# Kernel optimization log

Measured on AMD Instinct MI355X. Metric: run time of the kernel, lower is better.

The kernel has to match this reference:

```python
import jax, jax.numpy as jnp
import numpy as np
from jax import lax

B, NUM_HEADS, DIM_C, DIM_V = 8, 8, 768, 768
H = W = 56
HEAD_DIM = DIM_V // NUM_HEADS  # 96
STRIDE_Q = (1, 1)
STRIDE_KV = (2, 2)
REL_DIM = 2 * H - 1  # 111


def _ln(x, g, b, eps=1e-5):
    m = jnp.mean(x, axis=-1, keepdims=True)
    v = jnp.var(x, axis=-1, keepdims=True)
    return (x - m) * lax.rsqrt(v + eps) * g + b


def _pool(t, w, g, b, hw, stride):
    # t: [B, nH, 1+H*W, C]; depthwise 3x3 conv pooling (padding 1), cls token bypasses conv,
    # LayerNorm applied to the full (cls + pooled) tensor, matching attention_pool.
    cls_tok, sp = t[:, :, :1], t[:, :, 1:]
    b_, nh, L, c = sp.shape
    h, wdt = hw
    sp = sp.reshape(b_ * nh, h, wdt, c)
    sp = lax.conv_general_dilated(sp, w, stride, [(1, 1), (1, 1)],
                                  dimension_numbers=('NHWC', 'HWIO', 'NHWC'),
                                  feature_group_count=c)
    ho, wo = sp.shape[1], sp.shape[2]
    sp = sp.reshape(b_, nh, ho * wo, c)
    out = _ln(jnp.concatenate([cls_tok, sp], axis=2), g, b)
    return out, (ho, wo)


def _rel_idx(q_s, k_s):
    q_ratio = max(k_s / q_s, 1.0)
    k_ratio = max(q_s / k_s, 1.0)
    d = np.arange(q_s)[:, None] * q_ratio - np.arange(k_s)[None, :] * k_ratio + (k_s - 1) * k_ratio
    return d.astype(np.int64)


def setup_inputs() -> dict:
    key = jax.random.key(0)
    ks = jax.random.split(key, 8)
    N = H * W + 1
    return {
        'x': jax.random.normal(ks[0], (B, N, DIM_C), jnp.float32),
        'qkv_w': jax.random.normal(ks[1], (DIM_C, 3 * DIM_V), jnp.float32) * 0.02,
        'qkv_b': jnp.zeros((3 * DIM_V,), jnp.float32),
        'pool_q_w': jax.random.normal(ks[2], (3, 3, 1, HEAD_DIM), jnp.float32) * 0.1,
        'pool_k_w': jax.random.normal(ks[3], (3, 3, 1, HEAD_DIM), jnp.float32) * 0.1,
        'pool_v_w': jax.random.normal(ks[4], (3, 3, 1, HEAD_DIM), jnp.float32) * 0.1,
        'nq_g': jnp.ones((HEAD_DIM,), jnp.float32), 'nq_b': jnp.zeros((HEAD_DIM,), jnp.float32),
        'nk_g': jnp.ones((HEAD_DIM,), jnp.float32), 'nk_b': jnp.zeros((HEAD_DIM,), jnp.float32),
        'nv_g': jnp.ones((HEAD_DIM,), jnp.float32), 'nv_b': jnp.zeros((HEAD_DIM,), jnp.float32),
        'rel_pos_h': jax.random.normal(ks[5], (REL_DIM, HEAD_DIM), jnp.float32) * 0.02,
        'rel_pos_w': jax.random.normal(ks[6], (REL_DIM, HEAD_DIM), jnp.float32) * 0.02,
        'hw_h': H,
        'hw_w': W,
    }


def reference(x, qkv_w, qkv_b, pool_q_w, pool_k_w, pool_v_w,
              nq_g, nq_b, nk_g, nk_b, nv_g, nv_b,
              rel_pos_h, rel_pos_w, hw_h, hw_w):
    b, n, _ = x.shape
    qkv = (x @ qkv_w + qkv_b).reshape(b, n, 3, NUM_HEADS, HEAD_DIM).transpose(2, 0, 3, 1, 4)
    q, k, v = qkv[0], qkv[1], qkv[2]  # each [B, nH, N, head_dim]
    q, q_shape = _pool(q, pool_q_w, nq_g, nq_b, (hw_h, hw_w), STRIDE_Q)
    k, k_shape = _pool(k, pool_k_w, nk_g, nk_b, (hw_h, hw_w), STRIDE_KV)
    v, _ = _pool(v, pool_v_w, nv_g, nv_b, (hw_h, hw_w), STRIDE_KV)
    scale = HEAD_DIM ** -0.5
    attn = jnp.einsum('bhqc,bhkc->bhqk', q * scale, k)  # [B, nH, Nq, Nk]
    qh, qw = q_shape
    kh, kw = k_shape
    Rh = rel_pos_h[_rel_idx(qh, kh)]  # [qh, kh, C]
    Rw = rel_pos_w[_rel_idx(qw, kw)]  # [qw, kw, C]
    r_q = q[:, :, 1:].reshape(b, NUM_HEADS, qh, qw, HEAD_DIM)
    rel_h = jnp.einsum('byhwc,hkc->byhwk', r_q, Rh)
    rel_w = jnp.einsum('byhwc,wkc->byhwk', r_q, Rw)
    sp = attn[:, :, 1:, 1:].reshape(b, NUM_HEADS, qh, qw, kh, kw)
    sp = sp + rel_h[..., None] + rel_w[..., None, :]
    attn = attn.at[:, :, 1:, 1:].set(sp.reshape(b, NUM_HEADS, qh * qw, kh * kw))
    attn = jax.nn.softmax(attn, axis=-1)
    out = jnp.einsum('bhqk,bhkc->bhqc', attn, v)
    out = out + q  # residual pooling
    return out.transpose(0, 2, 1, 3).reshape(b, -1, DIM_V)
```

## Files before the change

### kernel.cpp

```cpp
#include <hip/hip_runtime.h>
#include <hip/hip_bf16.h>

typedef __hip_bfloat16 bf16;
typedef __attribute__((ext_vector_type(8))) short s16x8;
typedef __attribute__((ext_vector_type(4))) short s16x4;
typedef __attribute__((ext_vector_type(4))) float f32x4;

#define BATCH 8
#define NH 8
#define NTOK 3137
#define HD 96
#define HH 56
#define WW 56
#define NKEY 785
#define DIMC 768
#define DIM3 2304
#define MROWS (BATCH * NTOK)

__device__ __forceinline__ float b2f(bf16 x) { return __bfloat162float(x); }
__device__ __forceinline__ bf16 f2b(float x) { return __float2bfloat16(x); }
__device__ __forceinline__ float s2f(short s) {
  return __uint_as_float(((uint32_t)(uint16_t)s) << 16);
}
__device__ __forceinline__ short f2bs(float x) {
  bf16 h = __float2bfloat16(x);
  short s; __builtin_memcpy(&s, &h, 2); return s;
}
__device__ __forceinline__ void gload_lds16(const void* g, void* l) {
  __builtin_amdgcn_global_load_lds(
      (const __attribute__((address_space(1))) void*)g,
      (__attribute__((address_space(3))) void*)l, 16, 0, 0);
}
__device__ __forceinline__ int xcd_swz(int bid, int nwg) {
  int q = nwg >> 3, r = nwg & 7;
  int xcd = bid & 7, idx = bid >> 3;
  return (xcd < r ? xcd * (q + 1) : r * (q + 1) + (xcd - r) * q) + idx;
}

__global__ __launch_bounds__(256) void k_cvtX(const float* __restrict__ X,
                                              bf16* __restrict__ Xb, int n4) {
  for (int i = blockIdx.x * blockDim.x + threadIdx.x; i < n4;
       i += gridDim.x * blockDim.x) {
    float4 v = reinterpret_cast<const float4*>(X)[i];
    ushort4 o;
    o.x = (unsigned short)f2bs(v.x); o.y = (unsigned short)f2bs(v.y);
    o.z = (unsigned short)f2bs(v.z); o.w = (unsigned short)f2bs(v.w);
    reinterpret_cast<ushort4*>(Xb)[i] = o;
  }
}

__global__ __launch_bounds__(256) void k_cvtW(const float* __restrict__ W,
                                              bf16* __restrict__ WbT) {
  __shared__ float T[64][65];
  const int n0 = blockIdx.x * 64;
  const int k0 = blockIdx.y * 64;
  const int tid = threadIdx.x;
#pragma unroll
  for (int i = 0; i < 16; i++) {
    int e = tid + i * 256;
    int r = e >> 6, c = e & 63;
    T[r][c] = W[(size_t)(k0 + r) * DIM3 + n0 + c];
  }
  __syncthreads();
#pragma unroll
  for (int i = 0; i < 16; i++) {
    int e = tid + i * 256;
    int r = e >> 6, c = e & 63;
    WbT[(size_t)(n0 + r) * DIMC + k0 + c] = f2b(T[c][r]);
  }
}

__global__ __launch_bounds__(256) void k_cvtRel(const float* __restrict__ relHt,
                                                const float* __restrict__ relWt,
                                                bf16* __restrict__ Brel) {
  int i = blockIdx.x * 256 + threadIdx.x;
  if (i >= 5376) return;
  int elem = i * 4;
  int row = elem / HD, c = elem % HD;
  float4 v = {0.f, 0.f, 0.f, 0.f};
  if (row < 111) v = *(const float4*)(relHt + (size_t)row * HD + c);
  else if (row >= 112 && row < 223) v = *(const float4*)(relWt + (size_t)(row - 112) * HD + c);
  short4 o;
  o.x = f2bs(v.x); o.y = f2bs(v.y); o.z = f2bs(v.z); o.w = f2bs(v.w);
  *(short4*)((short*)Brel + elem) = o;
}

#define QKV_NBX 18
#define QKV_NBY 197
#define QKV_NWG (QKV_NBX * QKV_NBY)

__global__ __launch_bounds__(256, 4) void k_qkv_mfma(
    const bf16* __restrict__ Xb, const bf16* __restrict__ WbT,
    const float* __restrict__ bias,
    bf16* __restrict__ Q, bf16* __restrict__ K, bf16* __restrict__ V) {
  __shared__ __align__(16) short LB[17408];
  const int tid = threadIdx.x;
  const int wid = tid >> 6, lane = tid & 63;
  const int g = lane >> 4, kl = lane & 15;
  const int wm = wid >> 1, wn = wid & 1;
  const int lin = xcd_swz(blockIdx.x, QKV_NWG);
  const int row0 = (lin / QKV_NBX) * 128;
  const int col0 = (lin % QKV_NBX) * 128;

  auto stage = [&](int k0, int buf) {
#pragma unroll
    for (int r = 0; r < 2; r++) {
      int slotb = r * 256 + wid * 64;
      int slot = slotb + lane;
      int sg = slot >> 7, sm = slot & 127;
      int mm = row0 + sm; if (mm > MROWS - 1) mm = MROWS - 1;
      gload_lds16(Xb + (size_t)mm * DIMC + k0 + sg * 8, &LB[buf * 4096 + (slotb << 3)]);
      gload_lds16(WbT + (size_t)(col0 + sm) * DIMC + k0 + sg * 8,
                  &LB[8192 + buf * 4096 + (slotb << 3)]);
    }
  };

  f32x4 acc[4][4] = {};

  stage(0, 0);
  __syncthreads();

  for (int it = 0; it < 24; it++) {
    const int buf = it & 1;
    if (it < 23) stage((it + 1) * 32, buf ^ 1);

    s16x8 af[4], bf[4];
#pragma unroll
    for (int i = 0; i < 4; i++)
      af[i] = *(const s16x8*)&LB[buf * 4096 + (((g << 7) + wm * 64 + i * 16 + kl) << 3)];
#pragma unroll
    for (int j = 0; j < 4; j++)
      bf[j] = *(const s16x8*)&LB[8192 + buf * 4096 + (((g << 7) + wn * 64 + j * 16 + kl) << 3)];
    __builtin_amdgcn_s_setprio(1);
#pragma unroll
    for (int i = 0; i < 4; i++)
#pragma unroll
      for (int j = 0; j < 4; j++)
        acc[i][j] = __builtin_amdgcn_mfma_f32_16x16x32_bf16(af[i], bf[j], acc[i][j], 0, 0, 0);
    __builtin_amdgcn_s_setprio(0);
    __syncthreads();
  }

#pragma unroll
  for (int i = 0; i < 4; i++)
#pragma unroll
    for (int j = 0; j < 4; j++) {
      int n = wn * 64 + j * 16 + kl;
      float bv = bias[col0 + n];
#pragma unroll
      for (int r = 0; r < 4; r++) {
        int m = wm * 64 + i * 16 + g * 4 + r;
        LB[m * 136 + n] = f2bs(acc[i][j][r] + bv);
      }
    }
  __syncthreads();
#pragma unroll
  for (int cc8 = 0; cc8 < 8; cc8++) {
    int ch = tid + cc8 * 256;
    int m = ch >> 4, cc = ch & 15;
    int M = row0 + m;
    if (M < MROWS) {
      int ncol = col0 + cc * 8;
      int s = ncol / DIMC, rr = ncol % DIMC;
      int h = rr / HD, c = rr % HD;
      int b = M / NTOK, nt = M % NTOK;
      bf16* dst = (s == 0) ? Q : (s == 1) ? K : V;
      *(uint4*)(dst + (((size_t)b * NH + h) * NTOK + nt) * HD + c) =
          *(const uint4*)&LB[m * 136 + cc * 8];
    }
  }
}

template <int STRIDE, int OH_, int OW_>
__global__ __launch_bounds__(256) void k_pool(
    const bf16* __restrict__ raw, const float* __restrict__ wgt,
    const float* __restrict__ gam, const float* __restrict__ bet,
    bf16* __restrict__ out) {
  const int ntok = OH_ * OW_ + 1;
  const int ngrp = (ntok + 3) / 4;
  const int bid = xcd_swz(blockIdx.x, 64 * ngrp);
  const int grp = bid % ngrp;
  const int bh = bid / ngrp;
  const int wid = threadIdx.x >> 6, lane = threadIdx.x & 63;
  const int t = grp * 4 + wid;
  if (t >= ntok) return;
  const bf16* src = raw + (size_t)bh * NTOK * HD;
  const int c2 = lane * 2;

  float v0 = 0.f, v1 = 0.f;
  if (lane < 48) {
    if (t == 0) {
      ushort2 u = *(const ushort2*)(src + c2);
      v0 = s2f((short)u.x); v1 = s2f((short)u.y);
    } else {
      int oy = (t - 1) / OW_, ox = (t - 1) % OW_;
#pragma unroll
      for (int dy = 0; dy < 3; dy++) {
        int iy = oy * STRIDE + dy - 1;
        if (iy < 0 || iy >= HH) continue;
#pragma unroll
        for (int dx = 0; dx < 3; dx++) {
          int ix = ox * STRIDE + dx - 1;
          if (ix < 0 || ix >= WW) continue;
          ushort2 u = *(const ushort2*)(src + (size_t)(1 + iy * WW + ix) * HD + c2);
          float2 w = *(const float2*)(wgt + (dy * 3 + dx) * HD + c2);
          v0 += s2f((short)u.x) * w.x;
          v1 += s2f((short)u.y) * w.y;
        }
      }
    }
  }
  float s = v0 + v1;
  float s2 = v0 * v0 + v1 * v1;
#pragma unroll
  for (int o = 32; o > 0; o >>= 1) {
    s += __shfl_xor(s, o);
    s2 += __shfl_xor(s2, o);
  }
  float mean = s * (1.f / 96.f);
  float var = s2 * (1.f / 96.f) - mean * mean;
  float rstd = rsqrtf(var + 1e-5f);

  if (lane < 48) {
    float2 gm = *(const float2*)(gam + c2);
    float2 bt = *(const float2*)(bet + c2);
    ushort2 o2;
    o2.x = (unsigned short)f2bs((v0 - mean) * rstd * gm.x + bt.x);
    o2.y = (unsigned short)f2bs((v1 - mean) * rstd * gm.y + bt.y);
    *(ushort2*)(out + ((size_t)bh * ntok + t) * HD + c2) = o2;
  }
}

#define KS_OFF 0
#define VS_OFF 8192
#define RHT_OFF 14528
#define RWT_OFF 16432
#define PS_OFF 18336

__global__ __launch_bounds__(256, 4) void k_attn(
    const bf16* __restrict__ Qp, const bf16* __restrict__ Kp,
    const bf16* __restrict__ Vp, const bf16* __restrict__ BrelG,
    float* __restrict__ out) {
  __shared__ __align__(16) short LB[20384];

  const int bid = blockIdx.x;
  const int swz = (bid & 7) * 400 + (bid >> 3);
  const int bh = swz / 50, qt = swz % 50;
  const int qbase = qt * 64;
  const int tid = threadIdx.x, wid = tid >> 6, lane = tid & 63;
  const int g = lane >> 4, kl = lane & 15;
  const int bb = bh >> 3, hh = bh & 7;
  const float scale = 0.10206207261596575f;

  const bf16* Qbh = Qp + (size_t)bh * NTOK * HD;
  const bf16* Kbh = Kp + (size_t)bh * NKEY * HD;
  const bf16* Vbh = Vp + (size_t)bh * NKEY * HD;

  s16x8 qf[3];
  {
    int qg = qbase + wid * 16 + kl; if (qg > NTOK - 1) qg = NTOK - 1;
    const bf16* qptr = Qbh + (size_t)qg * HD;
#pragma unroll
    for (int f = 0; f < 3; f++)
      qf[f] = *(const s16x8*)(qptr + f * 32 + g * 8);
  }

  {
    short* SfH = &LB[0];
    short* SfW = &LB[7168];
    f32x4 accH[7], accW[7];
#pragma unroll
    for (int cf = 0; cf < 7; cf++) {
      accH[cf] = (f32x4){0.f, 0.f, 0.f, 0.f};
      accW[cf] = (f32x4){0.f, 0.f, 0.f, 0.f};
    }
#pragma unroll
    for (int cf = 0; cf < 7; cf++) {
#pragma unroll
      for (int kb = 0; kb < 3; kb++) {
        s16x8 bh_ = *(const s16x8*)((const short*)BrelG + (cf * 16 + kl) * 96 + kb * 32 + g * 8);
        s16x8 bw_ = *(const s16x8*)((const short*)BrelG + (112 + cf * 16 + kl) * 96 + kb * 32 + g * 8);
        accH[cf] = __builtin_amdgcn_mfma_f32_16x16x32_bf16(qf[kb], bh_, accH[cf], 0, 0, 0);
        accW[cf] = __builtin_amdgcn_mfma_f32_16x16x32_bf16(qf[kb], bw_, accW[cf], 0, 0, 0);
      }
    }
#pragma unroll
    for (int cf = 0; cf < 7; cf++)
#pragma unroll
      for (int r = 0; r < 4; r++) {
        int row = wid * 16 + g * 4 + r;
        SfH[row * 112 + cf * 16 + kl] = f2bs(accH[cf][r]);
        SfW[row * 112 + cf * 16 + kl] = f2bs(accW[cf][r]);
      }
    __syncthreads();
    for (int i = tid; i < 1792; i += 256) {
      int ql = i / 28, j = i % 28;
      int qg = qbase + ql; if (qg > NTOK - 1) qg = NTOK - 1;
      int qy, qx;
      if (qg < 1) { qy = 0; qx = 0; } else { qy = (qg - 1) / WW; qx = (qg - 1) % WW; }
      int ih = qy - 2 * j + 54; ih = ih < 0 ? 0 : (ih > 110 ? 110 : ih);
      int iw = qx - 2 * j + 54; iw = iw < 0 ? 0 : (iw > 110 ? 110 : iw);
      LB[RHT_OFF + j * 68 + ql] = SfH[ql * 112 + ih];
      LB[RWT_OFF + j * 68 + ql] = SfW[ql * 112 + iw];
    }
    __syncthreads();
  }

  s16x8 ones;
#pragma unroll
  for (int e = 0; e < 8; e++) ones[e] = (short)0x3F80;

  int kd0, vd0, go0, cs0, kd1, vd1, go1, cs1;
  {
    int kk = tid / 12, ch = tid % 12;
    kd0 = kk * 128 + ((ch ^ (kk & 7)) << 3);
    vd0 = (ch >> 1) * 528 + kk * 16 + ((ch & 1) << 3);
    go0 = kk * 96 + ch * 8;
    cs0 = (kk > 16) ? (kk - 16) * 96 : 0;
    int idx = 256 + tid;
    kk = idx / 12; ch = idx % 12;
    kd1 = kk * 128 + ((ch ^ (kk & 7)) << 3);
    vd1 = (ch >> 1) * 528 + kk * 16 + ((ch & 1) << 3);
    go1 = kk * 96 + ch * 8;
    cs1 = (kk > 16) ? (kk - 16) * 96 : 0;
  }

  auto stage = [&](int t, int buf) {
    short* ksb = &LB[KS_OFF + buf * 4096];
    short* vsb = &LB[VS_OFF + buf * 3168];
    int a0 = go0 - ((t == 24) ? cs0 : 0);
    uint4 ku = *(const uint4*)((const short*)Kbh + a0);
    uint4 vu = *(const uint4*)((const short*)Vbh + a0);
    *(uint4*)&ksb[kd0] = ku;
    *(uint4*)&vsb[vd0] = vu;
    go0 += 32 * 96;
    if (tid < 128) {
      int a1 = go1 - ((t == 24) ? cs1 : 0);
      uint4 ku1 = *(const uint4*)((const short*)Kbh + a1);
      uint4 vu1 = *(const uint4*)((const short*)Vbh + a1);
      *(uint4*)&ksb[kd1] = ku1;
      *(uint4*)&vsb[vd1] = vu1;
      go1 += 32 * 96;
    }
  };

  stage(0, 0);
  __syncthreads();

  f32x4 o[7];
#pragma unroll
  for (int cb = 0; cb < 7; cb++) o[cb] = (f32x4){0.f, 0.f, 0.f, 0.f};

  int kx0 = kl - 1;
  int ky0 = 0;
  int kx1 = (15 + kl) % 28;
  int ky1 = (15 + kl) / 28;
  const int qlb = wid * 16 + g * 4;

  for (int t = 0; t < 25; t++) {
    const int buf = t & 1;
    if (t < 24) stage(t + 1, buf ^ 1);

    const short* ksb = &LB[KS_OFF + buf * 4096];
    f32x4 s0 = (f32x4){0.f, 0.f, 0.f, 0.f};
    f32x4 s1 = (f32x4){0.f, 0.f, 0.f, 0.f};
    __builtin_amdgcn_s_setprio(1);
#pragma unroll
    for (int f = 0; f < 3; f++) {
      int ch = f * 4 + g;
      int r0 = kl, r1 = 16 + kl;
      s16x8 kf0 = *(const s16x8*)&ksb[r0 * 128 + ((ch ^ (r0 & 7)) << 3)];
      s16x8 kf1 = *(const s16x8*)&ksb[r1 * 128 + ((ch ^ (r1 & 7)) << 3)];
      s0 = __builtin_amdgcn_mfma_f32_16x16x32_bf16(qf[f], kf0, s0, 0, 0, 0);
      s1 = __builtin_amdgcn_mfma_f32_16x16x32_bf16(qf[f], kf1, s1, 0, 0, 0);
    }
    __builtin_amdgcn_s_setprio(0);

    const int k0g = t * 32 + kl;
    const int k1g = k0g + 16;
    int kxu0 = kx0 < 0 ? 0 : kx0;
    int kyu1 = ky1 > 27 ? 27 : ky1;
    s16x4 rh0 = *(const s16x4*)&LB[RHT_OFF + ky0 * 68 + qlb];
    s16x4 rw0 = *(const s16x4*)&LB[RWT_OFF + kxu0 * 68 + qlb];
    s16x4 rh1 = *(const s16x4*)&LB[RHT_OFF + kyu1 * 68 + qlb];
    s16x4 rw1 = *(const s16x4*)&LB[RWT_OFF + kx1 * 68 + qlb];

    float p0[4], p1[4];
#pragma unroll
    for (int r = 0; r < 4; r++) {
      int qg = qbase + qlb + r;
      float rel0 = (qg > 0 && k0g > 0) ? s2f(rh0[r]) + s2f(rw0[r]) : 0.f;
      float rel1 = (qg > 0) ? s2f(rh1[r]) + s2f(rw1[r]) : 0.f;
      float lg0 = s0[r] * scale + rel0;
      float lg1 = (k1g < NKEY) ? (s1[r] * scale + rel1) : -1e30f;
      p0[r] = __expf(lg0);
      p1[r] = __expf(lg1);
    }
    kx0 += 4; ky0 += 1; if (kx0 >= 28) { kx0 -= 28; ky0 += 1; }
    kx1 += 4; ky1 += 1; if (kx1 >= 28) { kx1 -= 28; ky1 += 1; }

    short* pw = &LB[PS_OFF + wid * 512];
    s16x4 pk0, pk1;
#pragma unroll
    for (int r = 0; r < 4; r++) { pk0[r] = f2bs(p0[r]); pk1[r] = f2bs(p1[r]); }
    *(s16x4*)(pw + kl * 16 + g * 4) = pk0;
    *(s16x4*)(pw + (16 + kl) * 16 + g * 4) = pk1;
    __builtin_amdgcn_sched_barrier(0);
    uint32_t pbase = (uint32_t)(size_t)pw + (uint32_t)(g * 256 + kl * 8);
    s16x4 pt0, pt1;
    asm volatile("ds_read_b64_tr_b16 %0, %1" : "=v"(pt0) : "v"(pbase));
    asm volatile("ds_read_b64_tr_b16 %0, %1 offset:128" : "=v"(pt1) : "v"(pbase));

    uint32_t vbase = (uint32_t)(size_t)&LB[VS_OFF + buf * 3168] + (uint32_t)(g * 256 + kl * 8);
    s16x4 tv[12];
#pragma unroll
    for (int cb = 0; cb < 6; cb++) {
      uint32_t va = vbase + cb * 1056;
      asm volatile("ds_read_b64_tr_b16 %0, %1" : "=v"(tv[2 * cb]) : "v"(va));
      asm volatile("ds_read_b64_tr_b16 %0, %1 offset:128" : "=v"(tv[2 * cb + 1]) : "v"(va));
    }
    asm volatile("s_waitcnt lgkmcnt(0)" ::: "memory");
    __builtin_amdgcn_sched_barrier(0);

    s16x8 pa = __builtin_shufflevector(pt0, pt1, 0, 1, 2, 3, 4, 5, 6, 7);
    __builtin_amdgcn_s_setprio(1);
    o[6] = __builtin_amdgcn_mfma_f32_16x16x32_bf16(pa, ones, o[6], 0, 0, 0);
#pragma unroll
    for (int cb = 0; cb < 6; cb++) {
      s16x8 vf = __builtin_shufflevector(tv[2 * cb], tv[2 * cb + 1], 0, 1, 2, 3, 4, 5, 6, 7);
      o[cb] = __builtin_amdgcn_mfma_f32_16x16x32_bf16(pa, vf, o[cb], 0, 0, 0);
    }
    __builtin_amdgcn_s_setprio(0);
    __syncthreads();
  }

  float inv[4];
#pragma unroll
  for (int r = 0; r < 4; r++) inv[r] = 1.f / o[6][r];
#pragma unroll
  for (int cb = 0; cb < 6; cb++) {
#pragma unroll
    for (int r = 0; r < 4; r++) {
      int ql = qlb + r;
      int qg = qbase + ql;
      if (qg < NTOK) {
        int c = cb * 16 + kl;
        float val = o[cb][r] * inv[r] + b2f(Qbh[(size_t)qg * HD + c]);
        out[((size_t)bb * NTOK + qg) * 768 + hh * 96 + c] = val;
      }
    }
  }
}

extern "C" void kernel_launch(void* const* d_in, const int* in_sizes, int n_in,
                              void* d_out, int out_size, void* d_ws, size_t ws_size,
                              hipStream_t stream) {
  const float* x = (const float*)d_in[0];
  const float* qkv_w = (const float*)d_in[1];
  const float* qkv_b = (const float*)d_in[2];
  const float* pqw = (const float*)d_in[3];
  const float* pkw = (const float*)d_in[4];
  const float* pvw = (const float*)d_in[5];
  const float* nqg = (const float*)d_in[6];
  const float* nqb = (const float*)d_in[7];
  const float* nkg = (const float*)d_in[8];
  const float* nkb = (const float*)d_in[9];
  const float* nvg = (const float*)d_in[10];
  const float* nvb = (const float*)d_in[11];
  const float* relH = (const float*)d_in[12];
  const float* relW = (const float*)d_in[13];

  const size_t SZQ = (size_t)MROWS * DIMC;
  const size_t SZK = (size_t)BATCH * NH * NKEY * HD;
  const size_t SZR = (size_t)BATCH * NH * NTOK * 28;

  bf16* ws = (bf16*)d_ws;
  bf16* Xb   = (bf16*)d_out;
  bf16* rawV = (bf16*)d_out + SZQ;
  bf16* rawQ = ws;
  bf16* rawK = ws + SZQ;
  bf16* WbT  = ws + 2 * SZQ;
  bf16* poolK = ws + 2 * SZQ;
  bf16* poolV = poolK + SZK;
  bf16* poolQ = rawK;
  bf16* Brel = ws + 2 * SZR;
  float* out = (float*)d_out;

  k_cvtX<<<2048, 256, 0, stream>>>(x, Xb, (int)(SZQ / 4));
  k_cvtW<<<dim3(DIM3 / 64, DIMC / 64), 256, 0, stream>>>(qkv_w, WbT);

  k_qkv_mfma<<<QKV_NWG, 256, 0, stream>>>(Xb, WbT, qkv_b, rawQ, rawK, rawV);

  k_pool<2, 28, 28><<<64 * 197, 256, 0, stream>>>(rawK, pkw, nkg, nkb, poolK);
  k_pool<2, 28, 28><<<64 * 197, 256, 0, stream>>>(rawV, pvw, nvg, nvb, poolV);
  k_pool<1, 56, 56><<<64 * 785, 256, 0, stream>>>(rawQ, pqw, nqg, nqb, poolQ);

  k_cvtRel<<<21, 256, 0, stream>>>(relH, relW, Brel);

  k_attn<<<64 * 50, 256, 0, stream>>>(poolQ, poolK, poolV, Brel, out);
}
```

Before: 533.3 us.

## Merge conversion and pooling kernels, fold rel-pos conversion into attention

```diff
diff --git a/kernel.cpp b/kernel.cpp
--- a/kernel.cpp
+++ b/kernel.cpp
@@ -37,63 +37,48 @@
   return (xcd < r ? xcd * (q + 1) : r * (q + 1) + (xcd - r) * q) + idx;
 }
 
-__global__ __launch_bounds__(256) void k_cvtX(const float* __restrict__ X,
-                                              bf16* __restrict__ Xb, int n4) {
-  for (int i = blockIdx.x * blockDim.x + threadIdx.x; i < n4;
-       i += gridDim.x * blockDim.x) {
-    float4 v = reinterpret_cast<const float4*>(X)[i];
-    ushort4 o;
-    o.x = (unsigned short)f2bs(v.x); o.y = (unsigned short)f2bs(v.y);
-    o.z = (unsigned short)f2bs(v.z); o.w = (unsigned short)f2bs(v.w);
-    reinterpret_cast<ushort4*>(Xb)[i] = o;
-  }
-}
-
-__global__ __launch_bounds__(256) void k_cvtW(const float* __restrict__ W,
-                                              bf16* __restrict__ WbT) {
+__global__ __launch_bounds__(256) void k_cvtAll(
+    const float* __restrict__ X, bf16* __restrict__ Xb, int n4,
+    const float* __restrict__ W, bf16* __restrict__ WbT) {
   __shared__ float T[64][65];
-  const int n0 = blockIdx.x * 64;
-  const int k0 = blockIdx.y * 64;
+  const int bid = blockIdx.x;
   const int tid = threadIdx.x;
-#pragma unroll
-  for (int i = 0; i < 16; i++) {
-    int e = tid + i * 256;
-    int r = e >> 6, c = e & 63;
-    T[r][c] = W[(size_t)(k0 + r) * DIM3 + n0 + c];
-  }
-  __syncthreads();
-#pragma unroll
-  for (int i = 0; i < 16; i++) {
-    int e = tid + i * 256;
-    int r = e >> 6, c = e & 63;
-    WbT[(size_t)(n0 + r) * DIMC + k0 + c] = f2b(T[c][r]);
-  }
-}
-
-__global__ __launch_bounds__(256) void k_cvtRel(const float* __restrict__ relHt,
-                                                const float* __restrict__ relWt,
-                                                bf16* __restrict__ Brel) {
-  int i = blockIdx.x * 256 + threadIdx.x;
-  if (i >= 5376) return;
-  int elem = i * 4;
-  int row = elem / HD, c = elem % HD;
-  float4 v = {0.f, 0.f, 0.f, 0.f};
-  if (row < 111) v = *(const float4*)(relHt + (size_t)row * HD + c);
-  else if (row >= 112 && row < 223) v = *(const float4*)(relWt + (size_t)(row - 112) * HD + c);
-  short4 o;
-  o.x = f2bs(v.x); o.y = f2bs(v.y); o.z = f2bs(v.z); o.w = f2bs(v.w);
-  *(short4*)((short*)Brel + elem) = o;
+  if (bid < 432) {
+    const int n0 = (bid % 36) * 64;
+    const int k0 = (bid / 36) * 64;
+#pragma unroll
+    for (int i = 0; i < 16; i++) {
+      int e = tid + i * 256;
+      int r = e >> 6, c = e & 63;
+      T[r][c] = W[(size_t)(k0 + r) * DIM3 + n0 + c];
+    }
+    __syncthreads();
+#pragma unroll
+    for (int i = 0; i < 16; i++) {
+      int e = tid + i * 256;
+      int r = e >> 6, c = e & 63;
+      WbT[(size_t)(n0 + r) * DIMC + k0 + c] = f2b(T[c][r]);
+    }
+  } else {
+    for (int i = (bid - 432) * 256 + tid; i < n4; i += (2480 - 432) * 256) {
+      float4 v = reinterpret_cast<const float4*>(X)[i];
+      ushort4 o;
+      o.x = (unsigned short)f2bs(v.x); o.y = (unsigned short)f2bs(v.y);
+      o.z = (unsigned short)f2bs(v.z); o.w = (unsigned short)f2bs(v.w);
+      reinterpret_cast<ushort4*>(Xb)[i] = o;
+    }
+  }
 }
 
 #define QKV_NBX 18
 #define QKV_NBY 197
 #define QKV_NWG (QKV_NBX * QKV_NBY)
 
-__global__ __launch_bounds__(256, 4) void k_qkv_mfma(
+__global__ __launch_bounds__(256, 5) void k_qkv_mfma(
     const bf16* __restrict__ Xb, const bf16* __restrict__ WbT,
     const float* __restrict__ bias,
     bf16* __restrict__ Q, bf16* __restrict__ K, bf16* __restrict__ V) {
-  __shared__ __align__(16) short LB[17408];
+  __shared__ __align__(16) short LB[16384];
   const int tid = threadIdx.x;
   const int wid = tid >> 6, lane = tid & 63;
   const int g = lane >> 4, kl = lane & 15;
@@ -142,42 +127,112 @@
   }
 
 #pragma unroll
-  for (int i = 0; i < 4; i++)
-#pragma unroll
-    for (int j = 0; j < 4; j++) {
-      int n = wn * 64 + j * 16 + kl;
-      float bv = bias[col0 + n];
-#pragma unroll
-      for (int r = 0; r < 4; r++) {
-        int m = wm * 64 + i * 16 + g * 4 + r;
-        LB[m * 136 + n] = f2bs(acc[i][j][r] + bv);
+  for (int half = 0; half < 2; half++) {
+    __syncthreads();
+    if (wm == half) {
+#pragma unroll
+      for (int i = 0; i < 4; i++)
+#pragma unroll
+        for (int j = 0; j < 4; j++) {
+          int n = wn * 64 + j * 16 + kl;
+          float bv = bias[col0 + n];
+#pragma unroll
+          for (int r = 0; r < 4; r++) {
+            int m = i * 16 + g * 4 + r;
+            LB[m * 138 + n] = f2bs(acc[i][j][r] + bv);
+          }
+        }
+    }
+    __syncthreads();
+#pragma unroll
+    for (int cc4 = 0; cc4 < 4; cc4++) {
+      int ch = tid + cc4 * 256;
+      int m = ch >> 4, cc = ch & 15;
+      int M = row0 + half * 64 + m;
+      if (M < MROWS) {
+        int ncol = col0 + cc * 8;
+        int s = ncol / DIMC, rr = ncol % DIMC;
+        int h = rr / HD, c = rr % HD;
+        int b = M / NTOK, nt = M % NTOK;
+        bf16* dst = (s == 0) ? Q : (s == 1) ? K : V;
+        *(uint4*)(dst + (((size_t)b * NH + h) * NTOK + nt) * HD + c) =
+            *(const uint4*)&LB[m * 138 + cc * 8];
       }
     }
-  __syncthreads();
-#pragma unroll
-  for (int cc8 = 0; cc8 < 8; cc8++) {
-    int ch = tid + cc8 * 256;
-    int m = ch >> 4, cc = ch & 15;
-    int M = row0 + m;
-    if (M < MROWS) {
-      int ncol = col0 + cc * 8;
-      int s = ncol / DIMC, rr = ncol % DIMC;
-      int h = rr / HD, c = rr % HD;
-      int b = M / NTOK, nt = M % NTOK;
-      bf16* dst = (s == 0) ? Q : (s == 1) ? K : V;
-      *(uint4*)(dst + (((size_t)b * NH + h) * NTOK + nt) * HD + c) =
-          *(const uint4*)&LB[m * 136 + cc * 8];
-    }
-  }
-}
-
-template <int STRIDE, int OH_, int OW_>
-__global__ __launch_bounds__(256) void k_pool(
+  }
+}
+
+__global__ __launch_bounds__(256) void k_poolKV(
+    const bf16* __restrict__ rawK, const bf16* __restrict__ rawV,
+    const float* __restrict__ wk, const float* __restrict__ wv,
+    const float* __restrict__ gk, const float* __restrict__ bk,
+    const float* __restrict__ gv, const float* __restrict__ bv,
+    bf16* __restrict__ outK, bf16* __restrict__ outV) {
+  const int ntok = 785, ngrp = 197, nb = 64 * ngrp;
+  const bool isV = blockIdx.x >= nb;
+  const int bid = xcd_swz(isV ? blockIdx.x - nb : blockIdx.x, nb);
+  const bf16* raw = isV ? rawV : rawK;
+  const float* wgt = isV ? wv : wk;
+  const float* gam = isV ? gv : gk;
+  const float* bet = isV ? bv : bk;
+  bf16* out = isV ? outV : outK;
+  const int grp = bid % ngrp;
+  const int bh = bid / ngrp;
+  const int wid = threadIdx.x >> 6, lane = threadIdx.x & 63;
+  const int t = grp * 4 + wid;
+  if (t >= ntok) return;
+  const bf16* src = raw + (size_t)bh * NTOK * HD;
+  const int c2 = lane * 2;
+
+  float v0 = 0.f, v1 = 0.f;
+  if (lane < 48) {
+    if (t == 0) {
+      ushort2 u = *(const ushort2*)(src + c2);
+      v0 = s2f((short)u.x); v1 = s2f((short)u.y);
+    } else {
+      int oy = (t - 1) / 28, ox = (t - 1) % 28;
+#pragma unroll
+      for (int dy = 0; dy < 3; dy++) {
+        int iy = oy * 2 + dy - 1;
+        if (iy < 0 || iy >= HH) continue;
+#pragma unroll
+        for (int dx = 0; dx < 3; dx++) {
+          int ix = ox * 2 + dx - 1;
+          if (ix < 0 || ix >= WW) continue;
+          ushort2 u = *(const ushort2*)(src + (size_t)(1 + iy * WW + ix) * HD + c2);
+          float2 w = *(const float2*)(wgt + (dy * 3 + dx) * HD + c2);
+          v0 += s2f((short)u.x) * w.x;
+          v1 += s2f((short)u.y) * w.y;
+        }
+      }
+    }
+  }
+  float s = v0 + v1;
+  float s2 = v0 * v0 + v1 * v1;
+#pragma unroll
+  for (int o = 32; o > 0; o >>= 1) {
+    s += __shfl_xor(s, o);
+    s2 += __shfl_xor(s2, o);
+  }
+  float mean = s * (1.f / 96.f);
+  float var = s2 * (1.f / 96.f) - mean * mean;
+  float rstd = rsqrtf(var + 1e-5f);
+
+  if (lane < 48) {
+    float2 gm = *(const float2*)(gam + c2);
+    float2 bt = *(const float2*)(bet + c2);
+    ushort2 o2;
+    o2.x = (unsigned short)f2bs((v0 - mean) * rstd * gm.x + bt.x);
+    o2.y = (unsigned short)f2bs((v1 - mean) * rstd * gm.y + bt.y);
+    *(ushort2*)(out + ((size_t)bh * ntok + t) * HD + c2) = o2;
+  }
+}
+
+__global__ __launch_bounds__(256) void k_poolQ(
     const bf16* __restrict__ raw, const float* __restrict__ wgt,
     const float* __restrict__ gam, const float* __restrict__ bet,
     bf16* __restrict__ out) {
-  const int ntok = OH_ * OW_ + 1;
-  const int ngrp = (ntok + 3) / 4;
+  const int ntok = NTOK, ngrp = 785;
   const int bid = xcd_swz(blockIdx.x, 64 * ngrp);
   const int grp = bid % ngrp;
   const int bh = bid / ngrp;
@@ -193,14 +248,14 @@
       ushort2 u = *(const ushort2*)(src + c2);
       v0 = s2f((short)u.x); v1 = s2f((short)u.y);
     } else {
-      int oy = (t - 1) / OW_, ox = (t - 1) % OW_;
+      int oy = (t - 1) / WW, ox = (t - 1) % WW;
 #pragma unroll
       for (int dy = 0; dy < 3; dy++) {
-        int iy = oy * STRIDE + dy - 1;
+        int iy = oy + dy - 1;
         if (iy < 0 || iy >= HH) continue;
 #pragma unroll
         for (int dx = 0; dx < 3; dx++) {
-          int ix = ox * STRIDE + dx - 1;
+          int ix = ox + dx - 1;
           if (ix < 0 || ix >= WW) continue;
           ushort2 u = *(const ushort2*)(src + (size_t)(1 + iy * WW + ix) * HD + c2);
           float2 w = *(const float2*)(wgt + (dy * 3 + dx) * HD + c2);
@@ -239,8 +294,8 @@
 
 __global__ __launch_bounds__(256, 4) void k_attn(
     const bf16* __restrict__ Qp, const bf16* __restrict__ Kp,
-    const bf16* __restrict__ Vp, const bf16* __restrict__ BrelG,
-    float* __restrict__ out) {
+    const bf16* __restrict__ Vp, const float* __restrict__ relHt,
+    const float* __restrict__ relWt, float* __restrict__ out) {
   __shared__ __align__(16) short LB[20384];
 
   const int bid = blockIdx.x;
@@ -268,6 +323,7 @@
   {
     short* SfH = &LB[0];
     short* SfW = &LB[7168];
+    const int row =  0 * 0 + (0);
     f32x4 accH[7], accW[7];
 #pragma unroll
     for (int cf = 0; cf < 7; cf++) {
@@ -276,10 +332,24 @@
     }
 #pragma unroll
     for (int cf = 0; cf < 7; cf++) {
+      int rw_ = cf * 16 + kl;
+      bool valid = rw_ < 111;
 #pragma unroll
       for (int kb = 0; kb < 3; kb++) {
-        s16x8 bh_ = *(const s16x8*)((const short*)BrelG + (cf * 16 + kl) * 96 + kb * 32 + g * 8);
-        s16x8 bw_ = *(const s16x8*)((const short*)BrelG + (112 + cf * 16 + kl) * 96 + kb * 32 + g * 8);
+        s16x8 bh_, bw_;
+        if (valid) {
+          const float* ph = relHt + (size_t)rw_ * HD + kb * 32 + g * 8;
+          const float* pw2 = relWt + (size_t)rw_ * HD + kb * 32 + g * 8;
+          float4 h0 = *(const float4*)ph, h1 = *(const float4*)(ph + 4);
+          float4 w0 = *(const float4*)pw2, w1 = *(const float4*)(pw2 + 4);
+          bh_[0] = f2bs(h0.x); bh_[1] = f2bs(h0.y); bh_[2] = f2bs(h0.z); bh_[3] = f2bs(h0.w);
+          bh_[4] = f2bs(h1.x); bh_[5] = f2bs(h1.y); bh_[6] = f2bs(h1.z); bh_[7] = f2bs(h1.w);
+          bw_[0] = f2bs(w0.x); bw_[1] = f2bs(w0.y); bw_[2] = f2bs(w0.z); bw_[3] = f2bs(w0.w);
+          bw_[4] = f2bs(w1.x); bw_[5] = f2bs(w1.y); bw_[6] = f2bs(w1.z); bw_[7] = f2bs(w1.w);
+        } else {
+#pragma unroll
+          for (int e = 0; e < 8; e++) { bh_[e] = 0; bw_[e] = 0; }
+        }
         accH[cf] = __builtin_amdgcn_mfma_f32_16x16x32_bf16(qf[kb], bh_, accH[cf], 0, 0, 0);
         accW[cf] = __builtin_amdgcn_mfma_f32_16x16x32_bf16(qf[kb], bw_, accW[cf], 0, 0, 0);
       }
@@ -288,9 +358,9 @@
     for (int cf = 0; cf < 7; cf++)
 #pragma unroll
       for (int r = 0; r < 4; r++) {
-        int row = wid * 16 + g * 4 + r;
-        SfH[row * 112 + cf * 16 + kl] = f2bs(accH[cf][r]);
-        SfW[row * 112 + cf * 16 + kl] = f2bs(accW[cf][r]);
+        int rr = wid * 16 + g * 4 + r;
+        SfH[rr * 112 + cf * 16 + kl] = f2bs(accH[cf][r]);
+        SfW[rr * 112 + cf * 16 + kl] = f2bs(accW[cf][r]);
       }
     __syncthreads();
     for (int i = tid; i < 1792; i += 256) {
@@ -472,7 +542,6 @@
 
   const size_t SZQ = (size_t)MROWS * DIMC;
   const size_t SZK = (size_t)BATCH * NH * NKEY * HD;
-  const size_t SZR = (size_t)BATCH * NH * NTOK * 28;
 
   bf16* ws = (bf16*)d_ws;
   bf16* Xb   = (bf16*)d_out;
@@ -483,19 +552,15 @@
   bf16* poolK = ws + 2 * SZQ;
   bf16* poolV = poolK + SZK;
   bf16* poolQ = rawK;
-  bf16* Brel = ws + 2 * SZR;
   float* out = (float*)d_out;
 
-  k_cvtX<<<2048, 256, 0, stream>>>(x, Xb, (int)(SZQ / 4));
-  k_cvtW<<<dim3(DIM3 / 64, DIMC / 64), 256, 0, stream>>>(qkv_w, WbT);
+  k_cvtAll<<<2480, 256, 0, stream>>>(x, Xb, (int)(SZQ / 4), qkv_w, WbT);
 
   k_qkv_mfma<<<QKV_NWG, 256, 0, stream>>>(Xb, WbT, qkv_b, rawQ, rawK, rawV);
 
-  k_pool<2, 28, 28><<<64 * 197, 256, 0, stream>>>(rawK, pkw, nkg, nkb, poolK);
-  k_pool<2, 28, 28><<<64 * 197, 256, 0, stream>>>(rawV, pvw, nvg, nvb, poolV);
-  k_pool<1, 56, 56><<<64 * 785, 256, 0, stream>>>(rawQ, pqw, nqg, nqb, poolQ);
-
-  k_cvtRel<<<21, 256, 0, stream>>>(relH, relW, Brel);
-
-  k_attn<<<64 * 50, 256, 0, stream>>>(poolQ, poolK, poolV, Brel, out);
-}
+  k_poolKV<<<2 * 64 * 197, 256, 0, stream>>>(rawK, rawV, pkw, pvw,
+                                             nkg, nkb, nvg, nvb, poolK, poolV);
+  k_poolQ<<<64 * 785, 256, 0, stream>>>(rawQ, pqw, nqg, nqb, poolQ);
+
+  k_attn<<<64 * 50, 256, 0, stream>>>(poolQ, poolK, poolV, relH, relW, out);
+}
```

New measurement: 994.0 us. 86.4% more time.
